# Kernel optimization log

Hardware: AMD Instinct MI355X
Metric: run time of the kernel (lower is better)

The kernel has to match this reference:

```python
import jax, jax.numpy as jnp
import numpy as np

B, N, D = 8, 65536, 192
EPS = 1e-5  # matches cal_norm_batch eps

# corner offsets (i,j,k) in {0,1}^3, shape [2,2,2,3]
_OFFS = np.stack(np.meshgrid(np.arange(2), np.arange(2), np.arange(2), indexing='ij'), -1)


def setup_inputs() -> dict:
    key = jax.random.key(0)
    k1, k2 = jax.random.split(key)
    pss = jax.random.uniform(k1, (B, 3, N), jnp.float32)          # points in [0,1]^3
    sdf_grids = jax.random.normal(k2, (B, D, D, D), jnp.float32)  # per-batch SDF grids
    first = jnp.zeros((B, 3), jnp.float32)                        # grid origin
    coef = jnp.full((B, 3), float(D - 2), jnp.float32)            # 1/voxel_size
    max_limit = jnp.full((B, 3), float(D - 2), jnp.float32)       # keeps idx+1 <= D-1
    return {"pss": pss, "sdf_grids": sdf_grids, "first": first, "coef": coef, "max_limit": max_limit}


def reference(pss, sdf_grids, first, coef, max_limit):
    p = jnp.transpose(pss, (0, 2, 1))  # [B,N,3]
    f_full = jnp.clip(jnp.minimum((p - first[:, None, :]) * coef[:, None, :],
                                  max_limit[:, None, :]), 0.0)
    base = jnp.floor(f_full)
    frac = f_full - base               # [B,N,3] trilinear fractions
    idx8 = base.astype(jnp.int32)[:, :, None, None, None, :] + jnp.asarray(_OFFS, jnp.int32)  # [B,N,2,2,2,3]
    # 8-corner gather, per-batch grid
    corners = jax.vmap(lambda g, I: g[I[..., 0], I[..., 1], I[..., 2]])(sdf_grids, idx8)  # [B,N,2,2,2]
    fx, fy, fz = frac[..., 0], frac[..., 1], frac[..., 2]
    wx = jnp.stack([1 - fx, fx], -1)  # [B,N,2]
    wy = jnp.stack([1 - fy, fy], -1)
    wz = jnp.stack([1 - fz, fz], -1)
    # trilinear SDF value
    dss = jnp.einsum('bnijk,bni,bnj,bnk->bn', corners, wx, wy, wz)
    # finite-difference normals (interp3d_batch with grad=True along each axis)
    n_z = jnp.einsum('bnij,bni,bnj->bn', corners[..., 1] - corners[..., 0], wx, wy)
    n_y = jnp.einsum('bnik,bni,bnk->bn', corners[:, :, :, 1, :] - corners[:, :, :, 0, :], wx, wz)
    n_x = jnp.einsum('bnjk,bnj,bnk->bn', corners[:, :, 1] - corners[:, :, 0], wy, wz)
    n = jnp.stack([n_x, n_y, n_z], -1)  # [B,N,3]
    nss = n / jnp.clip(jnp.linalg.norm(n, axis=-1, keepdims=True), EPS)
    loss = -jnp.sum(jnp.minimum(dss, 0.0))
    return dss, nss, loss
```

## Files before the change

kernel.cpp:

```cpp
#include <hip/hip_runtime.h>

#define BB 8
#define NN 65536
#define DD 192
#define EPSV 1e-5f
#define NPTS (BB * NN)


__global__ __launch_bounds__(256) void tri_sdf_kernel(
    const float* __restrict__ pss,
    const float* __restrict__ grid,
    const float* __restrict__ first,
    const float* __restrict__ coef,
    const float* __restrict__ maxl,
    float* __restrict__ dss,
    float* __restrict__ nss,
    float* __restrict__ loss)
{
    const int vb = ((int)blockIdx.x & 7) * 256 + ((int)blockIdx.x >> 3);
    const int t  = vb * 256 + (int)threadIdx.x;
    const int b  = t >> 16;
    const int n  = t & (NN - 1);

    const float* pb = pss + (size_t)b * 3 * NN + n;
    const float px = pb[0];
    const float py = pb[NN];
    const float pz = pb[2 * NN];

    const float fx_full = fmaxf(fminf((px - first[3*b+0]) * coef[3*b+0], maxl[3*b+0]), 0.0f);
    const float fy_full = fmaxf(fminf((py - first[3*b+1]) * coef[3*b+1], maxl[3*b+1]), 0.0f);
    const float fz_full = fmaxf(fminf((pz - first[3*b+2]) * coef[3*b+2], maxl[3*b+2]), 0.0f);

    const int bx = (int)floorf(fx_full);
    const int by = (int)floorf(fy_full);
    const int bz = (int)floorf(fz_full);
    const float fx = fx_full - (float)bx;
    const float fy = fy_full - (float)by;
    const float fz = fz_full - (float)bz;

    const float* g = grid + (size_t)b * DD * DD * DD
                          + ((size_t)bx * DD + by) * DD + bz;
    const float c000 = g[0];
    const float c001 = g[1];
    const float c010 = g[DD];
    const float c011 = g[DD + 1];
    const float c100 = g[DD * DD];
    const float c101 = g[DD * DD + 1];
    const float c110 = g[DD * DD + DD];
    const float c111 = g[DD * DD + DD + 1];

    const float wx0 = 1.0f - fx, wx1 = fx;
    const float wy0 = 1.0f - fy, wy1 = fy;
    const float wz0 = 1.0f - fz, wz1 = fz;

    const float d00 = wz0 * c000 + wz1 * c001;
    const float d01 = wz0 * c010 + wz1 * c011;
    const float d10 = wz0 * c100 + wz1 * c101;
    const float d11 = wz0 * c110 + wz1 * c111;
    const float d0  = wy0 * d00 + wy1 * d01;
    const float d1  = wy0 * d10 + wy1 * d11;
    const float dv  = wx0 * d0 + wx1 * d1;

    const float nz = wx0 * (wy0 * (c001 - c000) + wy1 * (c011 - c010))
                   + wx1 * (wy0 * (c101 - c100) + wy1 * (c111 - c110));
    const float ny = wx0 * (wz0 * (c010 - c000) + wz1 * (c011 - c001))
                   + wx1 * (wz0 * (c110 - c100) + wz1 * (c111 - c101));
    const float nx = wy0 * (wz0 * (c100 - c000) + wz1 * (c101 - c001))
                   + wy1 * (wz0 * (c110 - c010) + wz1 * (c111 - c011));

    const float nrm = sqrtf(nx * nx + ny * ny + nz * nz);
    const float inv = 1.0f / fmaxf(nrm, EPSV);

    dss[t] = dv;
    float* np_ = nss + (size_t)t * 3;
    np_[0] = nx * inv;
    np_[1] = ny * inv;
    np_[2] = nz * inv;

    float lp = fminf(dv, 0.0f);
    #pragma unroll
    for (int off = 32; off > 0; off >>= 1)
        lp += __shfl_down(lp, off, 64);
    __shared__ float wsum[4];
    const int wid = threadIdx.x >> 6;
    if ((threadIdx.x & 63) == 0) wsum[wid] = lp;
    __syncthreads();
    if (threadIdx.x == 0)
        atomicAdd(loss, -(wsum[0] + wsum[1] + wsum[2] + wsum[3]));
}

extern "C" void kernel_launch(void* const* d_in, const int* in_sizes, int n_in,
                              void* d_out, int out_size, void* d_ws, size_t ws_size,
                              hipStream_t stream) {
    const float* pss   = (const float*)d_in[0];
    const float* grid  = (const float*)d_in[1];
    const float* first = (const float*)d_in[2];
    const float* coef  = (const float*)d_in[3];
    const float* maxl  = (const float*)d_in[4];

    float* out  = (float*)d_out;
    float* dss  = out;
    float* nss  = out + (size_t)BB * NN;
    float* loss = out + (size_t)4 * BB * NN;

    hipMemsetAsync(loss, 0, sizeof(float), stream);

    const int threads = 256;
    const int blocks  = NPTS / threads;
    tri_sdf_kernel<<<blocks, threads, 0, stream>>>(pss, grid, first, coef, maxl,
                                                   dss, nss, loss);
}
```

Before: 313.1 us.

## Process two points per thread and replace atomic loss with two-stage reduction

```diff
diff --git a/kernel.cpp b/kernel.cpp
--- a/kernel.cpp
+++ b/kernel.cpp
@@ -5,6 +5,7 @@
 #define DD 192
 #define EPSV 1e-5f
 #define NPTS (BB * NN)
+#define NBLK 1024
 
 
 __global__ __launch_bounds__(256) void tri_sdf_kernel(
@@ -15,69 +16,103 @@
     const float* __restrict__ maxl,
     float* __restrict__ dss,
     float* __restrict__ nss,
-    float* __restrict__ loss)
+    float* __restrict__ partial)
 {
-    const int vb = ((int)blockIdx.x & 7) * 256 + ((int)blockIdx.x >> 3);
-    const int t  = vb * 256 + (int)threadIdx.x;
-    const int b  = t >> 16;
-    const int n  = t & (NN - 1);
+    const int vb = ((int)blockIdx.x & 7) * 128 + ((int)blockIdx.x >> 3);
+    const int t0 = vb * 512 + (int)threadIdx.x;
+    const int b  = t0 >> 16;
+    const int n0 = t0 & (NN - 1);
 
-    const float* pb = pss + (size_t)b * 3 * NN + n;
-    const float px = pb[0];
-    const float py = pb[NN];
-    const float pz = pb[2 * NN];
+    const float* pb = pss + (size_t)b * 3 * NN + n0;
+    const float pxA = pb[0],        pxB = pb[256];
+    const float pyA = pb[NN],       pyB = pb[NN + 256];
+    const float pzA = pb[2 * NN],   pzB = pb[2 * NN + 256];
 
-    const float fx_full = fmaxf(fminf((px - first[3*b+0]) * coef[3*b+0], maxl[3*b+0]), 0.0f);
-    const float fy_full = fmaxf(fminf((py - first[3*b+1]) * coef[3*b+1], maxl[3*b+1]), 0.0f);
-    const float fz_full = fmaxf(fminf((pz - first[3*b+2]) * coef[3*b+2], maxl[3*b+2]), 0.0f);
+    const float f0x = first[3*b+0], f0y = first[3*b+1], f0z = first[3*b+2];
+    const float cfx = coef[3*b+0],  cfy = coef[3*b+1],  cfz = coef[3*b+2];
+    const float mlx = maxl[3*b+0],  mly = maxl[3*b+1],  mlz = maxl[3*b+2];
 
-    const int bx = (int)floorf(fx_full);
-    const int by = (int)floorf(fy_full);
-    const int bz = (int)floorf(fz_full);
-    const float fx = fx_full - (float)bx;
-    const float fy = fy_full - (float)by;
-    const float fz = fz_full - (float)bz;
+    const float FxA = fmaxf(fminf((pxA - f0x) * cfx, mlx), 0.0f);
+    const float FyA = fmaxf(fminf((pyA - f0y) * cfy, mly), 0.0f);
+    const float FzA = fmaxf(fminf((pzA - f0z) * cfz, mlz), 0.0f);
+    const float FxB = fmaxf(fminf((pxB - f0x) * cfx, mlx), 0.0f);
+    const float FyB = fmaxf(fminf((pyB - f0y) * cfy, mly), 0.0f);
+    const float FzB = fmaxf(fminf((pzB - f0z) * cfz, mlz), 0.0f);
 
-    const float* g = grid + (size_t)b * DD * DD * DD
-                          + ((size_t)bx * DD + by) * DD + bz;
-    const float c000 = g[0];
-    const float c001 = g[1];
-    const float c010 = g[DD];
-    const float c011 = g[DD + 1];
-    const float c100 = g[DD * DD];
-    const float c101 = g[DD * DD + 1];
-    const float c110 = g[DD * DD + DD];
-    const float c111 = g[DD * DD + DD + 1];
+    const int bxA = (int)floorf(FxA), byA = (int)floorf(FyA), bzA = (int)floorf(FzA);
+    const int bxB = (int)floorf(FxB), byB = (int)floorf(FyB), bzB = (int)floorf(FzB);
+    const float fxA = FxA - (float)bxA, fyA = FyA - (float)byA, fzA = FzA - (float)bzA;
+    const float fxB = FxB - (float)bxB, fyB = FyB - (float)byB, fzB = FzB - (float)bzB;
 
-    const float wx0 = 1.0f - fx, wx1 = fx;
-    const float wy0 = 1.0f - fy, wy1 = fy;
-    const float wz0 = 1.0f - fz, wz1 = fz;
+    const float* gbase = grid + (size_t)b * DD * DD * DD;
+    const float* gA = gbase + ((size_t)bxA * DD + byA) * DD + bzA;
+    const float* gB = gbase + ((size_t)bxB * DD + byB) * DD + bzB;
 
-    const float d00 = wz0 * c000 + wz1 * c001;
-    const float d01 = wz0 * c010 + wz1 * c011;
-    const float d10 = wz0 * c100 + wz1 * c101;
-    const float d11 = wz0 * c110 + wz1 * c111;
-    const float d0  = wy0 * d00 + wy1 * d01;
-    const float d1  = wy0 * d10 + wy1 * d11;
-    const float dv  = wx0 * d0 + wx1 * d1;
+    const float a000 = gA[0];
+    const float a001 = gA[1];
+    const float a010 = gA[DD];
+    const float a011 = gA[DD + 1];
+    const float a100 = gA[DD * DD];
+    const float a101 = gA[DD * DD + 1];
+    const float a110 = gA[DD * DD + DD];
+    const float a111 = gA[DD * DD + DD + 1];
+    const float b000 = gB[0];
+    const float b001 = gB[1];
+    const float b010 = gB[DD];
+    const float b011 = gB[DD + 1];
+    const float b100 = gB[DD * DD];
+    const float b101 = gB[DD * DD + 1];
+    const float b110 = gB[DD * DD + DD];
+    const float b111 = gB[DD * DD + DD + 1];
 
-    const float nz = wx0 * (wy0 * (c001 - c000) + wy1 * (c011 - c010))
-                   + wx1 * (wy0 * (c101 - c100) + wy1 * (c111 - c110));
-    const float ny = wx0 * (wz0 * (c010 - c000) + wz1 * (c011 - c001))
-                   + wx1 * (wz0 * (c110 - c100) + wz1 * (c111 - c101));
-    const float nx = wy0 * (wz0 * (c100 - c000) + wz1 * (c101 - c001))
-                   + wy1 * (wz0 * (c110 - c010) + wz1 * (c111 - c011));
+    float wx0 = 1.0f - fxA, wx1 = fxA;
+    float wy0 = 1.0f - fyA, wy1 = fyA;
+    float wz0 = 1.0f - fzA, wz1 = fzA;
 
-    const float nrm = sqrtf(nx * nx + ny * ny + nz * nz);
-    const float inv = 1.0f / fmaxf(nrm, EPSV);
+    float d00 = wz0 * a000 + wz1 * a001;
+    float d01 = wz0 * a010 + wz1 * a011;
+    float d10 = wz0 * a100 + wz1 * a101;
+    float d11 = wz0 * a110 + wz1 * a111;
+    const float dvA = wx0 * (wy0 * d00 + wy1 * d01) + wx1 * (wy0 * d10 + wy1 * d11);
 
-    dss[t] = dv;
-    float* np_ = nss + (size_t)t * 3;
-    np_[0] = nx * inv;
-    np_[1] = ny * inv;
-    np_[2] = nz * inv;
+    const float nzA = wx0 * (wy0 * (a001 - a000) + wy1 * (a011 - a010))
+                    + wx1 * (wy0 * (a101 - a100) + wy1 * (a111 - a110));
+    const float nyA = wx0 * (wz0 * (a010 - a000) + wz1 * (a011 - a001))
+                    + wx1 * (wz0 * (a110 - a100) + wz1 * (a111 - a101));
+    const float nxA = wy0 * (wz0 * (a100 - a000) + wz1 * (a101 - a001))
+                    + wy1 * (wz0 * (a110 - a010) + wz1 * (a111 - a011));
+    const float invA = 1.0f / fmaxf(sqrtf(nxA*nxA + nyA*nyA + nzA*nzA), EPSV);
 
-    float lp = fminf(dv, 0.0f);
+    wx0 = 1.0f - fxB; wx1 = fxB;
+    wy0 = 1.0f - fyB; wy1 = fyB;
+    wz0 = 1.0f - fzB; wz1 = fzB;
+
+    d00 = wz0 * b000 + wz1 * b001;
+    d01 = wz0 * b010 + wz1 * b011;
+    d10 = wz0 * b100 + wz1 * b101;
+    d11 = wz0 * b110 + wz1 * b111;
+    const float dvB = wx0 * (wy0 * d00 + wy1 * d01) + wx1 * (wy0 * d10 + wy1 * d11);
+
+    const float nzB = wx0 * (wy0 * (b001 - b000) + wy1 * (b011 - b010))
+                    + wx1 * (wy0 * (b101 - b100) + wy1 * (b111 - b110));
+    const float nyB = wx0 * (wz0 * (b010 - b000) + wz1 * (b011 - b001))
+                    + wx1 * (wz0 * (b110 - b100) + wz1 * (b111 - b101));
+    const float nxB = wy0 * (wz0 * (b100 - b000) + wz1 * (b101 - b001))
+                    + wy1 * (wz0 * (b110 - b010) + wz1 * (b111 - b011));
+    const float invB = 1.0f / fmaxf(sqrtf(nxB*nxB + nyB*nyB + nzB*nzB), EPSV);
+
+    dss[t0]       = dvA;
+    dss[t0 + 256] = dvB;
+    float* npA = nss + (size_t)t0 * 3;
+    npA[0] = nxA * invA;
+    npA[1] = nyA * invA;
+    npA[2] = nzA * invA;
+    float* npB = nss + (size_t)(t0 + 256) * 3;
+    npB[0] = nxB * invB;
+    npB[1] = nyB * invB;
+    npB[2] = nzB * invB;
+
+    float lp = fminf(dvA, 0.0f) + fminf(dvB, 0.0f);
     #pragma unroll
     for (int off = 32; off > 0; off >>= 1)
         lp += __shfl_down(lp, off, 64);
@@ -86,7 +121,24 @@
     if ((threadIdx.x & 63) == 0) wsum[wid] = lp;
     __syncthreads();
     if (threadIdx.x == 0)
-        atomicAdd(loss, -(wsum[0] + wsum[1] + wsum[2] + wsum[3]));
+        partial[blockIdx.x] = wsum[0] + wsum[1] + wsum[2] + wsum[3];
+}
+
+__global__ __launch_bounds__(256) void loss_reduce_kernel(
+    const float* __restrict__ partial, float* __restrict__ loss)
+{
+    const int tid = threadIdx.x;
+    float s = partial[tid] + partial[tid + 256]
+            + partial[tid + 512] + partial[tid + 768];
+    #pragma unroll
+    for (int off = 32; off > 0; off >>= 1)
+        s += __shfl_down(s, off, 64);
+    __shared__ float wsum[4];
+    const int wid = tid >> 6;
+    if ((tid & 63) == 0) wsum[wid] = s;
+    __syncthreads();
+    if (tid == 0)
+        loss[0] = -(wsum[0] + wsum[1] + wsum[2] + wsum[3]);
 }
 
 extern "C" void kernel_launch(void* const* d_in, const int* in_sizes, int n_in,
@@ -103,10 +155,9 @@
     float* nss  = out + (size_t)BB * NN;
     float* loss = out + (size_t)4 * BB * NN;
 
-    hipMemsetAsync(loss, 0, sizeof(float), stream);
+    float* partial = (float*)d_ws;
 
-    const int threads = 256;
-    const int blocks  = NPTS / threads;
-    tri_sdf_kernel<<<blocks, threads, 0, stream>>>(pss, grid, first, coef, maxl,
-                                                   dss, nss, loss);
+    tri_sdf_kernel<<<NBLK, 256, 0, stream>>>(pss, grid, first, coef, maxl,
+                                             dss, nss, partial);
+    loss_reduce_kernel<<<1, 256, 0, stream>>>(partial, loss);
 }
```

New measurement: 310.3 us. About the same (-0.9%).
